# Kernel optimization log

Measured on AMD Instinct MI355X. Metric: run time of the kernel, lower is better.

Reference implementation:

```python
import jax, jax.numpy as jnp
import numpy as np


def _get_pixel_value(img, x, y, z):
    # img: (B, D, H, W, C); x/y/z: int32 (B, Do, Ho, Wo)
    B = img.shape[0]
    b = jnp.arange(B, dtype=jnp.int32)[:, None, None, None]
    return img[b, z, y, x]  # (B, Do, Ho, Wo, C)


def _trilinear_sampler(img, xs, ys, zs):
    D, H, W = img.shape[1], img.shape[2], img.shape[3]
    max_x, max_y, max_z = W - 1, H - 1, D - 1
    # NOTE: original scales by (max-1), i.e. (dim-2) -- kept faithfully.
    xs = 0.5 * (xs + 1.0) * jnp.float32(max_x - 1)
    ys = 0.5 * (ys + 1.0) * jnp.float32(max_y - 1)
    zs = 0.5 * (zs + 1.0) * jnp.float32(max_z - 1)
    x0 = jnp.floor(xs).astype(jnp.int32); x1 = x0 + 1
    y0 = jnp.floor(ys).astype(jnp.int32); y1 = y0 + 1
    z0 = jnp.floor(zs).astype(jnp.int32); z1 = z0 + 1
    x0 = jnp.clip(x0, 0, max_x); x1 = jnp.clip(x1, 0, max_x)
    y0 = jnp.clip(y0, 0, max_y); y1 = jnp.clip(y1, 0, max_y)
    z0 = jnp.clip(z0, 0, max_z); z1 = jnp.clip(z1, 0, max_z)
    Ia = _get_pixel_value(img, x0, y0, z0)
    Ib = _get_pixel_value(img, x0, y1, z0)
    Ic = _get_pixel_value(img, x1, y0, z0)
    Id = _get_pixel_value(img, x1, y1, z0)
    Ie = _get_pixel_value(img, x0, y0, z1)
    If = _get_pixel_value(img, x0, y1, z1)
    Ig = _get_pixel_value(img, x1, y0, z1)
    Ih = _get_pixel_value(img, x1, y1, z1)
    x0f = x0.astype(jnp.float32); x1f = x1.astype(jnp.float32)
    y0f = y0.astype(jnp.float32); y1f = y1.astype(jnp.float32)
    z0f = z0.astype(jnp.float32); z1f = z1.astype(jnp.float32)
    wa = ((x1f - xs) * (y1f - ys) * (z1f - zs))[..., None]
    wb = ((x1f - xs) * (ys - y0f) * (z1f - zs))[..., None]
    wc = ((xs - x0f) * (y1f - ys) * (z1f - zs))[..., None]
    wd = ((xs - x0f) * (ys - y0f) * (z1f - zs))[..., None]
    we = ((x1f - xs) * (y1f - ys) * (zs - z0f))[..., None]
    wf = ((x1f - xs) * (ys - y0f) * (zs - z0f))[..., None]
    wg = ((xs - x0f) * (y1f - ys) * (zs - z0f))[..., None]
    wh = ((xs - x0f) * (ys - y0f) * (zs - z0f))[..., None]
    return (wa * Ia + wb * Ib + wc * Ic + wd * Id
            + we * Ie + wf * If + wg * Ig + wh * Ih)


def _affine_grid(depth, height, width, theta):
    d = jnp.linspace(-1.0, 1.0, depth, dtype=jnp.float32)
    h = jnp.linspace(-1.0, 1.0, height, dtype=jnp.float32)
    w = jnp.linspace(-1.0, 1.0, width, dtype=jnp.float32)
    # tf.meshgrid(h, d, w) (indexing='xy') -> outputs of shape (D, H, W):
    # x_t varies along H, z_t along D, y_t along W.
    z_t, x_t, y_t = jnp.meshgrid(d, h, w, indexing='ij')
    ones = jnp.ones_like(x_t)
    grid = jnp.stack([x_t.ravel(), y_t.ravel(), z_t.ravel(), ones.ravel()], axis=0)  # (4, N)
    batch_grids = jnp.einsum('bij,jn->bin', theta, grid)  # (B, 3, N)
    return batch_grids.reshape(theta.shape[0], 3, depth, height, width)


def reference(x, hw_d, hw_h, hw_w):
    B = x.shape[0]
    theta = jnp.tile(jnp.asarray([[[1, 0, 0, 0], [0, 1, 0, 0], [0, 0, 1, 0]]],
                                 dtype=jnp.float32), (B, 1, 1))
    gridout = _affine_grid(int(hw_d), int(hw_h), int(hw_w), theta)
    y_s = gridout[:, 0]
    x_s = gridout[:, 1]
    z_s = gridout[:, 2]
    return _trilinear_sampler(x, x_s, y_s, z_s)


def setup_inputs() -> dict:
    key = jax.random.key(0)
    x = jax.random.normal(key, (4, 64, 64, 64, 32), dtype=jnp.float32)
    return {"x": x, "hw_d": 64, "hw_h": 64, "hw_w": 64}
```

## Files before the change

kernel.cpp:

```cpp
#include <hip/hip_runtime.h>


#define BD 4
#define DD 64
#define HH 64
#define WW 64
#define CC 32
#define C4 (CC / 4)

__global__ __launch_bounds__(256) void trilerp_kernel(
    const float4* __restrict__ in, float4* __restrict__ out) {
    int t = blockIdx.x * blockDim.x + threadIdx.x;

    int cq  = t & (C4 - 1);
    int vox = t >> 3;
    int k = vox & 63;
    int j = (vox >> 6) & 63;
    int i = (vox >> 12) & 63;
    int b = vox >> 18;

    const float s = 62.0f / 63.0f;
    float xs = (float)k * s;
    float ys = (float)j * s;
    float zs = (float)i * s;

    int x0 = (int)xs;
    int y0 = (int)ys;
    int z0 = (int)zs;
    float fx = xs - (float)x0;
    float fy = ys - (float)y0;
    float fz = zs - (float)z0;
    int x1 = min(x0 + 1, WW - 1);
    int y1 = min(y0 + 1, HH - 1);
    int z1 = min(z0 + 1, DD - 1);

    int bb  = b << 21;
    int z0o = bb + (z0 << 15);
    int z1o = bb + (z1 << 15);
    int y0o = y0 << 9;
    int y1o = y1 << 9;
    int x0o = (x0 << 3) + cq;
    int x1o = (x1 << 3) + cq;

    float4 v000 = in[z0o + y0o + x0o];
    float4 v010 = in[z0o + y1o + x0o];
    float4 v001 = in[z0o + y0o + x1o];
    float4 v011 = in[z0o + y1o + x1o];
    float4 v100 = in[z1o + y0o + x0o];
    float4 v110 = in[z1o + y1o + x0o];
    float4 v101 = in[z1o + y0o + x1o];
    float4 v111 = in[z1o + y1o + x1o];

    float gx = 1.0f - fx, gy = 1.0f - fy, gz = 1.0f - fz;
    float wa = gx * gy * gz;
    float wb = gx * fy * gz;
    float wc = fx * gy * gz;
    float wd = fx * fy * gz;
    float we = gx * gy * fz;
    float wf = gx * fy * fz;
    float wg = fx * gy * fz;
    float wh = fx * fy * fz;

    float4 r;
    r.x = fmaf(v000.x, wa, fmaf(v010.x, wb, fmaf(v001.x, wc, fmaf(v011.x, wd,
          fmaf(v100.x, we, fmaf(v110.x, wf, fmaf(v101.x, wg, v111.x * wh)))))));
    r.y = fmaf(v000.y, wa, fmaf(v010.y, wb, fmaf(v001.y, wc, fmaf(v011.y, wd,
          fmaf(v100.y, we, fmaf(v110.y, wf, fmaf(v101.y, wg, v111.y * wh)))))));
    r.z = fmaf(v000.z, wa, fmaf(v010.z, wb, fmaf(v001.z, wc, fmaf(v011.z, wd,
          fmaf(v100.z, we, fmaf(v110.z, wf, fmaf(v101.z, wg, v111.z * wh)))))));
    r.w = fmaf(v000.w, wa, fmaf(v010.w, wb, fmaf(v001.w, wc, fmaf(v011.w, wd,
          fmaf(v100.w, we, fmaf(v110.w, wf, fmaf(v101.w, wg, v111.w * wh)))))));

    out[t] = r;
}

extern "C" void kernel_launch(void* const* d_in, const int* in_sizes, int n_in,
                              void* d_out, int out_size, void* d_ws, size_t ws_size,
                              hipStream_t stream) {
    const float4* in = (const float4*)d_in[0];
    float4* out = (float4*)d_out;

    const int total = BD * DD * HH * WW * C4;
    const int block = 256;
    const int grid = total / block;

    trilerp_kernel<<<grid, block, 0, stream>>>(in, out);
}
```

Measured before the change: 238.9 us.

## Compute two adjacent x outputs per thread to share corner loads

Each thread now produces two neighbouring output voxels along x. It loads three x-columns per (y,z) corner pair, 12 float4 loads instead of 16 for the two outputs, and picks per-output weights with a select depending on whether the second sample crosses a cell boundary. The upper-bound clamps are dropped because the fixed scale keeps indices in range, and a sched_barrier groups all loads ahead of the FMAs. This halves the thread count and cuts redundant gathers. Each store instruction now covers a strided rather than fully contiguous range, and register pressure per thread rises.

```diff
diff --git a/kernel.cpp b/kernel.cpp
--- a/kernel.cpp
+++ b/kernel.cpp
@@ -1,77 +1,83 @@
 #include <hip/hip_runtime.h>
 
 
-#define BD 4
-#define DD 64
-#define HH 64
-#define WW 64
-#define CC 32
-#define C4 (CC / 4)
+#define C4 8
 
-__global__ __launch_bounds__(256) void trilerp_kernel(
+__device__ __forceinline__ void fma4(float4& a, const float4 v, float w) {
+    a.x = fmaf(v.x, w, a.x);
+    a.y = fmaf(v.y, w, a.y);
+    a.z = fmaf(v.z, w, a.z);
+    a.w = fmaf(v.w, w, a.w);
+}
+
+__global__ __launch_bounds__(256) void trilerp2_kernel(
     const float4* __restrict__ in, float4* __restrict__ out) {
     int t = blockIdx.x * blockDim.x + threadIdx.x;
 
-    int cq  = t & (C4 - 1);
-    int vox = t >> 3;
-    int k = vox & 63;
-    int j = (vox >> 6) & 63;
-    int i = (vox >> 12) & 63;
-    int b = vox >> 18;
+    int cq = t & (C4 - 1);
+    int pv = t >> 3;
+    int kp = pv & 31;
+    int j  = (pv >> 5) & 63;
+    int i  = (pv >> 11) & 63;
+    int b  = pv >> 17;
 
     const float s = 62.0f / 63.0f;
-    float xs = (float)k * s;
-    float ys = (float)j * s;
-    float zs = (float)i * s;
+    int k0 = kp << 1;
+    float xs0 = (float)k0 * s;
+    float xs1 = (float)(k0 + 1) * s;
+    float ys  = (float)j * s;
+    float zs  = (float)i * s;
 
-    int x0 = (int)xs;
-    int y0 = (int)ys;
-    int z0 = (int)zs;
-    float fx = xs - (float)x0;
-    float fy = ys - (float)y0;
-    float fz = zs - (float)z0;
-    int x1 = min(x0 + 1, WW - 1);
-    int y1 = min(y0 + 1, HH - 1);
-    int z1 = min(z0 + 1, DD - 1);
+    int x00 = (int)xs0;
+    int x01 = (int)xs1;
+    int y0  = (int)ys;
+    int z0  = (int)zs;
+    float fx0 = xs0 - (float)x00;
+    float fx1 = xs1 - (float)x01;
+    float fy  = ys - (float)y0;
+    float fz  = zs - (float)z0;
+    float gy = 1.0f - fy, gz = 1.0f - fz;
 
-    int bb  = b << 21;
-    int z0o = bb + (z0 << 15);
-    int z1o = bb + (z1 << 15);
-    int y0o = y0 << 9;
-    int y1o = y1 << 9;
-    int x0o = (x0 << 3) + cq;
-    int x1o = (x1 << 3) + cq;
+    float w00 = gy * gz;
+    float w01 = fy * gz;
+    float w10 = gy * fz;
+    float w11 = fy * fz;
 
-    float4 v000 = in[z0o + y0o + x0o];
-    float4 v010 = in[z0o + y1o + x0o];
-    float4 v001 = in[z0o + y0o + x1o];
-    float4 v011 = in[z0o + y1o + x1o];
-    float4 v100 = in[z1o + y0o + x0o];
-    float4 v110 = in[z1o + y1o + x0o];
-    float4 v101 = in[z1o + y0o + x1o];
-    float4 v111 = in[z1o + y1o + x1o];
+    float a0 = 1.0f - fx0;
+    float a1 = fx0;
+    bool adv = x01 > x00;
+    float b0 = adv ? 0.0f        : (1.0f - fx1);
+    float b1 = adv ? (1.0f - fx1) : fx1;
+    float b2 = adv ? fx1         : 0.0f;
 
-    float gx = 1.0f - fx, gy = 1.0f - fy, gz = 1.0f - fz;
-    float wa = gx * gy * gz;
-    float wb = gx * fy * gz;
-    float wc = fx * gy * gz;
-    float wd = fx * fy * gz;
-    float we = gx * gy * fz;
-    float wf = gx * fy * fz;
-    float wg = fx * gy * fz;
-    float wh = fx * fy * fz;
+    int bb = b << 21;
+    const float4* r00 = in + bb + (z0 << 15)        + (y0 << 9)        + (x00 << 3) + cq;
+    const float4* r01 = in + bb + (z0 << 15)        + ((y0 + 1) << 9)  + (x00 << 3) + cq;
+    const float4* r10 = in + bb + ((z0 + 1) << 15)  + (y0 << 9)        + (x00 << 3) + cq;
+    const float4* r11 = in + bb + ((z0 + 1) << 15)  + ((y0 + 1) << 9)  + (x00 << 3) + cq;
 
-    float4 r;
-    r.x = fmaf(v000.x, wa, fmaf(v010.x, wb, fmaf(v001.x, wc, fmaf(v011.x, wd,
-          fmaf(v100.x, we, fmaf(v110.x, wf, fmaf(v101.x, wg, v111.x * wh)))))));
-    r.y = fmaf(v000.y, wa, fmaf(v010.y, wb, fmaf(v001.y, wc, fmaf(v011.y, wd,
-          fmaf(v100.y, we, fmaf(v110.y, wf, fmaf(v101.y, wg, v111.y * wh)))))));
-    r.z = fmaf(v000.z, wa, fmaf(v010.z, wb, fmaf(v001.z, wc, fmaf(v011.z, wd,
-          fmaf(v100.z, we, fmaf(v110.z, wf, fmaf(v101.z, wg, v111.z * wh)))))));
-    r.w = fmaf(v000.w, wa, fmaf(v010.w, wb, fmaf(v001.w, wc, fmaf(v011.w, wd,
-          fmaf(v100.w, we, fmaf(v110.w, wf, fmaf(v101.w, wg, v111.w * wh)))))));
+    float4 v00_0 = r00[0], v00_1 = r00[8], v00_2 = r00[16];
+    float4 v01_0 = r01[0], v01_1 = r01[8], v01_2 = r01[16];
+    float4 v10_0 = r10[0], v10_1 = r10[8], v10_2 = r10[16];
+    float4 v11_0 = r11[0], v11_1 = r11[8], v11_2 = r11[16];
+    __builtin_amdgcn_sched_barrier(0);
 
-    out[t] = r;
+    float4 acc0 = make_float4(0.f, 0.f, 0.f, 0.f);
+    float4 acc1 = make_float4(0.f, 0.f, 0.f, 0.f);
+
+    fma4(acc0, v00_0, w00 * a0);  fma4(acc0, v00_1, w00 * a1);
+    fma4(acc0, v01_0, w01 * a0);  fma4(acc0, v01_1, w01 * a1);
+    fma4(acc0, v10_0, w10 * a0);  fma4(acc0, v10_1, w10 * a1);
+    fma4(acc0, v11_0, w11 * a0);  fma4(acc0, v11_1, w11 * a1);
+
+    fma4(acc1, v00_0, w00 * b0);  fma4(acc1, v00_1, w00 * b1);  fma4(acc1, v00_2, w00 * b2);
+    fma4(acc1, v01_0, w01 * b0);  fma4(acc1, v01_1, w01 * b1);  fma4(acc1, v01_2, w01 * b2);
+    fma4(acc1, v10_0, w10 * b0);  fma4(acc1, v10_1, w10 * b1);  fma4(acc1, v10_2, w10 * b2);
+    fma4(acc1, v11_0, w11 * b0);  fma4(acc1, v11_1, w11 * b1);  fma4(acc1, v11_2, w11 * b2);
+
+    int o0 = (((((b << 6) + i) << 6) + j) << 6 | k0) * 8 + cq;
+    out[o0]     = acc0;
+    out[o0 + 8] = acc1;
 }
 
 extern "C" void kernel_launch(void* const* d_in, const int* in_sizes, int n_in,
@@ -80,9 +86,9 @@
     const float4* in = (const float4*)d_in[0];
     float4* out = (float4*)d_out;
 
-    const int total = BD * DD * HH * WW * C4;
+    const int total = 4 * 64 * 64 * 32 * C4;
     const int block = 256;
     const int grid = total / block;
 
-    trilerp_kernel<<<grid, block, 0, stream>>>(in, out);
+    trilerp2_kernel<<<grid, block, 0, stream>>>(in, out);
 }
```

Result: slower. 245.1 us (+2.6%).
